# Optimization experiments

Measured on AMD Instinct MI355X. Metric: run time of the kernel, lower is better.

## Reference

```python
import jax, jax.numpy as jnp
import numpy as np

B = 64        # graphs in batch
N = 512       # nodes per graph (equal-size graphs)
DEG = 16      # avg degree
D_IN = 512
D_OUT = 512
RATIO = 0.5
K = int(np.ceil(RATIO * N))  # nodes kept per graph by SAGPool
NUM_NODES = B * N


def setup_inputs() -> dict:
    key = jax.random.key(0)
    ks = jax.random.split(key, 12)
    e_per = N * DEG
    offs = (jnp.arange(B, dtype=jnp.int32) * N)[:, None]
    src = (jax.random.randint(ks[0], (B, e_per), 0, N, dtype=jnp.int32) + offs).reshape(-1)
    dst = (jax.random.randint(ks[1], (B, e_per), 0, N, dtype=jnp.int32) + offs).reshape(-1)
    x = jax.random.normal(ks[2], (NUM_NODES, D_IN), jnp.float32)
    sc = 0.05  # small init so relu/tanh stay in sane range
    return {
        'x': x,
        'src': src,
        'dst': dst,
        'W1': jax.random.normal(ks[3], (D_IN, D_OUT), jnp.float32) * sc,
        'b1': jnp.zeros((D_OUT,), jnp.float32),
        'W2': jax.random.normal(ks[4], (D_OUT, D_OUT), jnp.float32) * sc,
        'b2': jnp.zeros((D_OUT,), jnp.float32),
        'sW1': jax.random.normal(ks[5], (D_OUT, 1), jnp.float32) * sc,
        'sb1': jnp.zeros((1,), jnp.float32),
        'sW2': jax.random.normal(ks[6], (D_OUT, 1), jnp.float32) * sc,
        'sb2': jnp.zeros((1,), jnp.float32),
    }


def graph_conv(src, dst, x, W, b, n_nodes):
    """DGL GraphConv, norm='both': D_in^{-1/2} A D_out^{-1/2} x W + b.
    W applied before aggregation (mathematically identical, cheaper when out_dim small)."""
    ones = jnp.ones(src.shape[0], x.dtype)
    deg_out = jax.ops.segment_sum(ones, src, num_segments=n_nodes)
    deg_in = jax.ops.segment_sum(ones, dst, num_segments=n_nodes)
    norm_out = jnp.maximum(deg_out, 1.0) ** -0.5  # DGL clamps deg to min 1
    norm_in = jnp.maximum(deg_in, 1.0) ** -0.5
    h = (x @ W) * norm_out[:, None]               # [n, out]
    m = jax.ops.segment_sum(h[src], dst, num_segments=n_nodes)  # gather+scatter over edges
    return m * norm_in[:, None] + b


def reference(x, src, dst, W1, b1, W2, b2, sW1, sb1, sW2, sb2):
    n = NUM_NODES
    h = jax.nn.relu(graph_conv(src, dst, x, W1, b1, n))   # conv1 + relu, reshape(-1,512) is a no-op
    h = jax.nn.relu(graph_conv(src, dst, h, W2, b2, n))   # conv2 + relu
    # SAGPool: two GraphConv score layers, averaged
    s1 = graph_conv(src, dst, h, sW1, sb1, n)[:, 0]
    s2 = graph_conv(src, dst, h, sW2, sb2, n)[:, 0]
    score = 0.5 * (s1 + s2)                                # [B*N]
    _, top_idx = jax.lax.top_k(score.reshape(B, N), K)     # per-graph top-k, [B, K]
    perm = (top_idx + (jnp.arange(B, dtype=top_idx.dtype) * N)[:, None]).reshape(-1)  # global ids
    pooled = h[perm] * jnp.tanh(score[perm])[:, None]      # [B*K, D_OUT] gated gather
    pb = pooled.reshape(B, K, D_OUT)
    # readout: max || sum per graph
    g_out = jnp.concatenate([pb.max(axis=1), pb.sum(axis=1)], axis=-1)  # [B, 2*D_OUT]
    return pooled, g_out
```

## Files before the change

kernel.cpp:

```cpp
#include <hip/hip_runtime.h>
#include <math.h>

typedef unsigned short u16;
typedef __attribute__((ext_vector_type(8))) short bf16x8;
typedef __attribute__((ext_vector_type(4))) float f32x4;

#define NN 32768
#define EDGES 524288
#define NB 64
#define NPG 512
#define EPG 8192
#define KEEP 256
#define D 512

__device__ __forceinline__ float b2f(u16 h){ return __uint_as_float(((unsigned)h)<<16); }
__device__ __forceinline__ u16 f2b(float f){
  unsigned u = __float_as_uint(f);
  unsigned r = u + 0x7FFFu + ((u>>16)&1u);
  return (u16)(r>>16);
}

__device__ __forceinline__ void gload16(const void* g, void* l){
  __builtin_amdgcn_global_load_lds((const __attribute__((address_space(1))) void*)g,
                                   (__attribute__((address_space(3))) void*)l, 16, 0, 0);
}

__device__ __forceinline__ int flag_f32(const u16* __restrict__ xb, int tid){
  __shared__ int fl;
  if (tid < 64){
    u16 v0 = xb[tid*2], v1 = xb[tid*2+1];
    int c = ((((v0>>7)&0xFF) > 140) ? 1 : 0) + ((((v1>>7)&0xFF) > 140) ? 1 : 0);
    #pragma unroll
    for (int o=32; o>=1; o>>=1) c += __shfl_xor(c, o);
    if (tid == 0) fl = (c > 8) ? 1 : 0;
  }
  __syncthreads();
  return fl;
}

__global__ __launch_bounds__(512) void prep_kernel(
    const int* __restrict__ src, const int* __restrict__ dst,
    float* __restrict__ no, float* __restrict__ ni,
    int* __restrict__ rowp, int* __restrict__ csr,
    const void* __restrict__ x,
    const void* b1, const void* b2, const void* sW1v, const void* sW2v,
    const void* sb1, const void* sb2,
    float* b1c, float* b2c, float* sW1c, float* sW2c, float* sbc,
    const void* __restrict__ W1, const void* __restrict__ W2,
    u16* __restrict__ W1Th, u16* __restrict__ W1Tl,
    u16* __restrict__ W2Th, u16* __restrict__ W2Tl,
    u16* __restrict__ Xh, u16* __restrict__ Xl)
{
  __shared__ int sh_i[5][NPG];
  __shared__ float tile[32][33];
  int b = blockIdx.x, t = threadIdx.x;

  if (b < NB){
    int* dego = sh_i[0]; int* degi = sh_i[1]; int* s = sh_i[2];
    int* start = sh_i[3]; int* cur = sh_i[4];
    int g = b, n = t;
    dego[n] = 0; degi[n] = 0; cur[n] = 0;
    __syncthreads();
    int ebase = g*EPG;
    #pragma unroll
    for (int i = 0; i < 16; i++){
      int e = ebase + n + i*512;
      atomicAdd(&dego[src[e] & (NPG-1)], 1);
      atomicAdd(&degi[dst[e] & (NPG-1)], 1);
    }
    __syncthreads();
    int di = degi[n];
    s[n] = di;
    __syncthreads();
    for (int off=1; off<NPG; off<<=1){
      int val = (n>=off) ? s[n-off] : 0;
      __syncthreads();
      s[n] += val;
      __syncthreads();
    }
    int excl = s[n] - di;
    start[n] = excl;
    int a = dego[n]; if (a<1) a=1;
    int bb = di;     if (bb<1) bb=1;
    int v = g*NPG + n;
    no[v] = (float)(1.0/sqrt((double)a));
    ni[v] = (float)(1.0/sqrt((double)bb));
    rowp[v] = ebase + excl;
    if (g == NB-1 && n == NPG-1) rowp[NN] = EDGES;
    __syncthreads();
    #pragma unroll
    for (int i = 0; i < 16; i++){
      int e = ebase + n + i*512;
      int dl = dst[e] & (NPG-1);
      int pos = atomicAdd(&cur[dl], 1);
      csr[ebase + start[dl] + pos] = src[e];
    }
  } else if (b == NB){
    int f = flag_f32((const u16*)x, t);
    #define CV(p,i) (f ? ((const float*)(p))[i] : b2f(((const u16*)(p))[i]))
    b1c[t]  = CV(b1, t);
    b2c[t]  = CV(b2, t);
    sW1c[t] = CV(sW1v, t);
    sW2c[t] = CV(sW2v, t);
    if (t==0){ sbc[0] = CV(sb1,0); sbc[1] = CV(sb2,0); }
    #undef CV
  } else if (b < NB + 1 + 512){
    int f = flag_f32((const u16*)x, t);
    int id = b - (NB+1);
    const void* W = (id >> 8) ? W2 : W1;
    u16* WTh = (id >> 8) ? W2Th : W1Th;
    u16* WTl = (id >> 8) ? W2Tl : W1Tl;
    int rem = id & 255;
    int bx = (rem & 15)*32, by = (rem >> 4)*32;
    int tx = t & 31, ty = t >> 5;
    #pragma unroll
    for (int i=0;i<2;i++){
      size_t idx = (size_t)(by+ty+i*16)*D + bx+tx;
      tile[ty+i*16][tx] = f ? ((const float*)W)[idx] : b2f(((const u16*)W)[idx]);
    }
    __syncthreads();
    #pragma unroll
    for (int i=0;i<2;i++){
      float v = tile[tx][ty+i*16];
      u16 h = f2b(v);
      size_t o = (size_t)(bx+ty+i*16)*D + by+tx;
      WTh[o] = h;
      WTl[o] = f2b(v - b2f(h));
    }
  } else {
    int f = flag_f32((const u16*)x, t);
    int nblk = gridDim.x - (NB+1+512);
    int bid  = b - (NB+1+512);
    size_t stride = (size_t)nblk*512*4;
    for (size_t i = ((size_t)bid*512 + t)*4; i < (size_t)NN*D; i += stride){
      float v0,v1,v2,v3;
      if (f){
        float4 fv = *(const float4*)((const float*)x + i);
        v0=fv.x; v1=fv.y; v2=fv.z; v3=fv.w;
      } else {
        ushort4 uv = *(const ushort4*)((const u16*)x + i);
        v0=b2f(uv.x); v1=b2f(uv.y); v2=b2f(uv.z); v3=b2f(uv.w);
      }
      ushort4 hh, hl;
      hh.x=f2b(v0); hl.x=f2b(v0-b2f(hh.x));
      hh.y=f2b(v1); hl.y=f2b(v1-b2f(hh.y));
      hh.z=f2b(v2); hl.z=f2b(v2-b2f(hh.z));
      hh.w=f2b(v3); hl.w=f2b(v3-b2f(hh.w));
      *(ushort4*)(Xh+i) = hh;
      *(ushort4*)(Xl+i) = hl;
    }
  }
}


__device__ __forceinline__ void gemm_tile256(int id, int& brow, int& bcol){
  int xcd = id & 7, k = id >> 3;
  brow = (xcd + 8*(k >> 1)) * 256;
  bcol = (k & 1) * 256;
}

__global__ __launch_bounds__(512, 2) void gemm256(
    const u16* __restrict__ Ahg, const u16* __restrict__ Alg,
    const u16* __restrict__ BTh, const u16* __restrict__ BTl,
    float* __restrict__ C, const float* __restrict__ rowscale)
{
  __shared__ alignas(16) u16 lds[2][4][8192];
  int t = threadIdx.x;
  int brow, bcol;
  gemm_tile256(blockIdx.x, brow, bcol);
  int wid = t>>6, lane = t&63;
  int wr = wid>>2, wc = wid&3;
  int q = lane>>4, r = lane&15;
  f32x4 acc[8][4] = {};

  int c0 = wid*128 + lane, c1 = c0 + 64;
  int q0 = c0>>8, r0 = c0&255, q1 = c1>>8, r1 = c1&255;
  const u16* sA0h = Ahg + (size_t)(brow+r0)*D + q0*8;
  const u16* sA1h = Ahg + (size_t)(brow+r1)*D + q1*8;
  const u16* sA0l = Alg + (size_t)(brow+r0)*D + q0*8;
  const u16* sA1l = Alg + (size_t)(brow+r1)*D + q1*8;
  const u16* sB0h = BTh + (size_t)(bcol+r0)*D + q0*8;
  const u16* sB1h = BTh + (size_t)(bcol+r1)*D + q1*8;
  const u16* sB0l = BTl + (size_t)(bcol+r0)*D + q0*8;
  const u16* sB1l = BTl + (size_t)(bcol+r1)*D + q1*8;

  #define STAGEK(B, KT) { int ko = (KT)*32; \
    gload16(sA0h+ko, &lds[B][0][c0*8]); gload16(sA1h+ko, &lds[B][0][c1*8]); \
    gload16(sA0l+ko, &lds[B][1][c0*8]); gload16(sA1l+ko, &lds[B][1][c1*8]); \
    gload16(sB0h+ko, &lds[B][2][c0*8]); gload16(sB1h+ko, &lds[B][2][c1*8]); \
    gload16(sB0l+ko, &lds[B][3][c0*8]); gload16(sB1l+ko, &lds[B][3][c1*8]); }

  STAGEK(0, 0)
  asm volatile("s_waitcnt vmcnt(0)" ::: "memory");
  __syncthreads();
  int cur = 0;
  for (int kt=0; kt<16; kt++){
    if (kt < 15) STAGEK(cur^1, kt+1)
    bf16x8 fbh[4], fbl[4];
    #pragma unroll
    for (int n=0;n<4;n++){
      fbh[n] = *(const bf16x8*)(&lds[cur][2][(q*256 + wc*64 + n*16 + r)*8]);
      fbl[n] = *(const bf16x8*)(&lds[cur][3][(q*256 + wc*64 + n*16 + r)*8]);
    }
    __builtin_amdgcn_s_setprio(1);
    #pragma unroll
    for (int m=0;m<8;m++){
      bf16x8 fah = *(const bf16x8*)(&lds[cur][0][(q*256 + wr*128 + m*16 + r)*8]);
      bf16x8 fal = *(const bf16x8*)(&lds[cur][1][(q*256 + wr*128 + m*16 + r)*8]);
      #pragma unroll
      for (int n=0;n<4;n++){
        acc[m][n] = __builtin_amdgcn_mfma_f32_16x16x32_bf16(fah, fbh[n], acc[m][n], 0,0,0);
        acc[m][n] = __builtin_amdgcn_mfma_f32_16x16x32_bf16(fah, fbl[n], acc[m][n], 0,0,0);
        acc[m][n] = __builtin_amdgcn_mfma_f32_16x16x32_bf16(fal, fbh[n], acc[m][n], 0,0,0);
      }
    }
    __builtin_amdgcn_s_setprio(0);
    asm volatile("s_waitcnt vmcnt(0)" ::: "memory");
    __syncthreads();
    cur ^= 1;
  }
  #undef STAGEK

  #pragma unroll
  for (int m=0;m<8;m++){
    int rowb = brow + wr*128 + m*16 + q*4;
    #pragma unroll
    for (int n=0;n<4;n++){
      int col = bcol + wc*64 + n*16 + r;
      #pragma unroll
      for (int g=0; g<4; g++){
        int row = rowb + g;
        C[(size_t)row*D + col] = acc[m][n][g] * rowscale[row];
      }
    }
  }
}


__global__ __launch_bounds__(256) void agg_kernel(
    const float* __restrict__ Y, const int* __restrict__ rowp,
    const int* __restrict__ csr, const float* __restrict__ ni,
    const float* __restrict__ bias,
    u16* __restrict__ Hh, u16* __restrict__ Hl,
    const float* __restrict__ sW1, const float* __restrict__ sW2,
    float* __restrict__ t1, float* __restrict__ t2, int mode)
{
  int i = blockIdx.x;
  int xcd = i & 7, j = i >> 3;
  int half = threadIdx.x >> 7;
  int t = threadIdx.x & 127;
  int lane = threadIdx.x & 63;
  int v = (xcd + 8*(j >> 8))*NPG + ((j & 255)*2 + half);
  int rp0 = rowp[v], rp1 = rowp[v+1];
  const float4* Yv = (const float4*)Y;
  float4 a = {0.f,0.f,0.f,0.f};
  for (int eb = rp0; eb < rp1; eb += 64){
    int cnt = rp1 - eb; if (cnt > 64) cnt = 64;
    int idx = (lane < cnt) ? csr[eb + lane] : 0;
    int e = 0;
    for (; e+8 <= cnt; e += 8){
      int u0 = __shfl(idx, e),   u1 = __shfl(idx, e+1);
      int u2 = __shfl(idx, e+2), u3 = __shfl(idx, e+3);
      int u4 = __shfl(idx, e+4), u5 = __shfl(idx, e+5);
      int u6 = __shfl(idx, e+6), u7 = __shfl(idx, e+7);
      float4 y0 = Yv[(size_t)u0*128 + t];
      float4 y1 = Yv[(size_t)u1*128 + t];
      float4 y2 = Yv[(size_t)u2*128 + t];
      float4 y3 = Yv[(size_t)u3*128 + t];
      float4 y4 = Yv[(size_t)u4*128 + t];
      float4 y5 = Yv[(size_t)u5*128 + t];
      float4 y6 = Yv[(size_t)u6*128 + t];
      float4 y7 = Yv[(size_t)u7*128 + t];
      a.x += ((y0.x + y1.x) + (y2.x + y3.x)) + ((y4.x + y5.x) + (y6.x + y7.x));
      a.y += ((y0.y + y1.y) + (y2.y + y3.y)) + ((y4.y + y5.y) + (y6.y + y7.y));
      a.z += ((y0.z + y1.z) + (y2.z + y3.z)) + ((y4.z + y5.z) + (y6.z + y7.z));
      a.w += ((y0.w + y1.w) + (y2.w + y3.w)) + ((y4.w + y5.w) + (y6.w + y7.w));
    }
    for (; e+4 <= cnt; e += 4){
      int u0 = __shfl(idx, e),   u1 = __shfl(idx, e+1);
      int u2 = __shfl(idx, e+2), u3 = __shfl(idx, e+3);
      float4 y0 = Yv[(size_t)u0*128 + t];
      float4 y1 = Yv[(size_t)u1*128 + t];
      float4 y2 = Yv[(size_t)u2*128 + t];
      float4 y3 = Yv[(size_t)u3*128 + t];
      a.x += (y0.x + y1.x) + (y2.x + y3.x);
      a.y += (y0.y + y1.y) + (y2.y + y3.y);
      a.z += (y0.z + y1.z) + (y2.z + y3.z);
      a.w += (y0.w + y1.w) + (y2.w + y3.w);
    }
    for (; e < cnt; e++){
      int u = __shfl(idx, e);
      float4 y = Yv[(size_t)u*128 + t];
      a.x += y.x; a.y += y.y; a.z += y.z; a.w += y.w;
    }
  }
  float w = ni[v];
  float4 b4 = ((const float4*)bias)[t];
  float4 rr;
  rr.x = fmaxf(a.x*w + b4.x, 0.f);
  rr.y = fmaxf(a.y*w + b4.y, 0.f);
  rr.z = fmaxf(a.z*w + b4.z, 0.f);
  rr.w = fmaxf(a.w*w + b4.w, 0.f);

  if (mode == 0){
    ushort4 hh, hl;
    hh.x = f2b(rr.x); hl.x = f2b(rr.x - b2f(hh.x));
    hh.y = f2b(rr.y); hl.y = f2b(rr.y - b2f(hh.y));
    hh.z = f2b(rr.z); hl.z = f2b(rr.z - b2f(hh.z));
    hh.w = f2b(rr.w); hl.w = f2b(rr.w - b2f(hh.w));
    *(ushort4*)(Hh + (size_t)v*D + t*4) = hh;
    *(ushort4*)(Hl + (size_t)v*D + t*4) = hl;
  } else {
    ushort4 hb;
    hb.x = f2b(rr.x); hb.y = f2b(rr.y); hb.z = f2b(rr.z); hb.w = f2b(rr.w);
    *(ushort4*)(Hh + (size_t)v*D + t*4) = hb;
    float4 w1 = ((const float4*)sW1)[t];
    float4 w2 = ((const float4*)sW2)[t];
    float p1 = rr.x*w1.x + rr.y*w1.y + rr.z*w1.z + rr.w*w1.w;
    float p2 = rr.x*w2.x + rr.y*w2.y + rr.z*w2.z + rr.w*w2.w;
    #pragma unroll
    for (int off=32; off>=1; off>>=1){
      p1 += __shfl_xor(p1, off);
      p2 += __shfl_xor(p2, off);
    }
    __shared__ float red1[4], red2[4];
    int wv = threadIdx.x>>6;
    if (lane==0){ red1[wv] = p1; red2[wv] = p2; }
    __syncthreads();
    if (t==0){
      t1[v] = red1[half*2] + red1[half*2+1];
      t2[v] = red2[half*2] + red2[half*2+1];
    }
  }
}


__global__ __launch_bounds__(512) void scoretopk_kernel(
    const float* __restrict__ t1, const float* __restrict__ t2,
    const int* __restrict__ rowp, const int* __restrict__ csr,
    const float* __restrict__ no, const float* __restrict__ ni,
    const float* __restrict__ sbc,
    int* __restrict__ perm, float* __restrict__ gate)
{
  __shared__ unsigned long long key[NPG];
  __shared__ float scl[NPG];
  int g = blockIdx.x, n = threadIdx.x;
  int v = g*NPG + n;
  double a1 = 0.0, a2 = 0.0;
  int rp1 = rowp[v+1];
  for (int e=rowp[v]; e<rp1; e++){
    int u = csr[e];
    double w = (double)no[u];
    a1 += (double)t1[u]*w;
    a2 += (double)t2[u]*w;
  }
  double wi = (double)ni[v];
  double s1 = a1*wi + (double)sbc[0];
  double s2 = a2*wi + (double)sbc[1];
  float s = (float)(0.5*(s1+s2));
  scl[n] = s;
  unsigned u = __float_as_uint(s);
  u = (u & 0x80000000u) ? ~u : (u | 0x80000000u);
  unsigned kd = ~u;
  key[n] = ((unsigned long long)kd<<32) | (unsigned)n;
  __syncthreads();
  for (int k=2; k<=NPG; k<<=1){
    for (int j=k>>1; j>0; j>>=1){
      int ixj = n ^ j;
      if (ixj > n){
        unsigned long long a = key[n], b = key[ixj];
        bool up = ((n & k) == 0);
        if ((a > b) == up){ key[n] = b; key[ixj] = a; }
      }
      __syncthreads();
    }
  }
  if (n < KEEP){
    int idx = (int)(key[n] & 0xFFFFFFFFull);
    perm[g*KEEP + n] = g*NPG + idx;
    gate[g*KEEP + n] = tanhf(scl[idx]);
  }
}


__global__ __launch_bounds__(256) void readout_kernel(const u16* __restrict__ Hb,
    const int* __restrict__ perm, const float* __restrict__ gate,
    float* __restrict__ outp, float* __restrict__ gmx, float* __restrict__ gsm)
{
  __shared__ float4 redmx[128], redsm[128];
  int b = blockIdx.x;
  int g = b >> 3, seg = b & 7;
  int t = threadIdx.x, half = t >> 7, c = t & 127;
  float4 mx = {-INFINITY,-INFINITY,-INFINITY,-INFINITY};
  float4 sm = {0.f,0.f,0.f,0.f};
  int base = seg*32;
  for (int rI = base + half; rI < base + 32; rI += 2){
    int node = perm[g*KEEP + rI];
    float gt = gate[g*KEEP + rI];
    ushort4 hv = *(const ushort4*)(Hb + (size_t)node*D + c*4);
    float4 vv;
    vv.x = b2f(hv.x)*gt; vv.y = b2f(hv.y)*gt;
    vv.z = b2f(hv.z)*gt; vv.w = b2f(hv.w)*gt;
    ((float4*)(outp + (size_t)(g*KEEP + rI)*D))[c] = vv;
    mx.x = fmaxf(mx.x, vv.x); mx.y = fmaxf(mx.y, vv.y);
    mx.z = fmaxf(mx.z, vv.z); mx.w = fmaxf(mx.w, vv.w);
    sm.x += vv.x; sm.y += vv.y; sm.z += vv.z; sm.w += vv.w;
  }
  if (half == 1){ redmx[c] = mx; redsm[c] = sm; }
  __syncthreads();
  if (half == 0){
    float4 omx = redmx[c], osm = redsm[c];
    mx.x = fmaxf(mx.x, omx.x); mx.y = fmaxf(mx.y, omx.y);
    mx.z = fmaxf(mx.z, omx.z); mx.w = fmaxf(mx.w, omx.w);
    sm.x += osm.x; sm.y += osm.y; sm.z += osm.z; sm.w += osm.w;
    ((float4*)(gmx + (size_t)b*512))[c] = mx;
    ((float4*)(gsm + (size_t)b*512))[c] = sm;
  }
}


__global__ __launch_bounds__(512) void combine_kernel(const float* __restrict__ gmx,
    const float* __restrict__ gsm, float* __restrict__ outg)
{
  int g = blockIdx.x, d = threadIdx.x;
  float mx = -INFINITY, sm = 0.f;
  #pragma unroll
  for (int s=0; s<8; s++){
    mx = fmaxf(mx, gmx[(size_t)(g*8+s)*512 + d]);
    sm += gsm[(size_t)(g*8+s)*512 + d];
  }
  outg[(size_t)g*1024 + d] = mx;
  outg[(size_t)g*1024 + 512 + d] = sm;
}


extern "C" void kernel_launch(void* const* d_in, const int* in_sizes, int n_in,
                              void* d_out, int out_size, void* d_ws, size_t ws_size,
                              hipStream_t stream)
{
  (void)in_sizes; (void)n_in; (void)out_size; (void)ws_size;
  const void* x   = d_in[0];
  const int* src  = (const int*)d_in[1];
  const int* dst  = (const int*)d_in[2];
  const void* W1  = d_in[3];
  const void* b1  = d_in[4];
  const void* W2  = d_in[5];
  const void* b2  = d_in[6];
  const void* sW1 = d_in[7];
  const void* sb1 = d_in[8];
  const void* sW2 = d_in[9];
  const void* sb2 = d_in[10];
  float* out = (float*)d_out;

  char* ws = (char*)d_ws;
  size_t off = 0;
  auto alloc = [&](size_t bytes){ void* p = ws + off; off += (bytes + 255) & ~(size_t)255; return p; };
  float* no     = (float*)alloc((size_t)NN*4);
  float* ni     = (float*)alloc((size_t)NN*4);
  int*   rowp   = (int*)  alloc((size_t)(NN+1)*4);
  float* t1     = (float*)alloc((size_t)NN*4);
  float* t2     = (float*)alloc((size_t)NN*4);
  int*   perm   = (int*)  alloc((size_t)NB*KEEP*4);
  float* gate   = (float*)alloc((size_t)NB*KEEP*4);
  float* b1c    = (float*)alloc((size_t)D*4);
  float* b2c    = (float*)alloc((size_t)D*4);
  float* sW1c   = (float*)alloc((size_t)D*4);
  float* sW2c   = (float*)alloc((size_t)D*4);
  float* sbc    = (float*)alloc(2*4);
  float* gmx    = (float*)alloc((size_t)512*512*4);
  float* gsm    = (float*)alloc((size_t)512*512*4);
  u16*   W1Th   = (u16*)  alloc((size_t)D*D*2);
  u16*   W1Tl   = (u16*)  alloc((size_t)D*D*2);
  u16*   W2Th   = (u16*)  alloc((size_t)D*D*2);
  u16*   W2Tl   = (u16*)  alloc((size_t)D*D*2);
  int*   csr    = (int*)  alloc((size_t)EDGES*4);
  u16*   Hh     = (u16*)  alloc((size_t)NN*D*2);
  u16*   Hl     = (u16*)  alloc((size_t)NN*D*2);
  float* Y      = (float*)alloc((size_t)NN*D*4);
  u16*   Xh     = (u16*)  alloc((size_t)NN*D*2);
  u16*   Xl     = (u16*)  alloc((size_t)NN*D*2);
  u16*   Hb     = Hh;

  prep_kernel<<<2048, 512, 0, stream>>>(src, dst, no, ni, rowp, csr, x,
                                        b1, b2, sW1, sW2, sb1, sb2,
                                        b1c, b2c, sW1c, sW2c, sbc,
                                        W1, W2, W1Th, W1Tl, W2Th, W2Tl, Xh, Xl);

  gemm256<<<256, 512, 0, stream>>>(Xh, Xl, W1Th, W1Tl, Y, no);
  agg_kernel<<<NN/2, 256, 0, stream>>>(Y, rowp, csr, ni, b1c, Hh, Hl,
                                       nullptr, nullptr, nullptr, nullptr, 0);
  gemm256<<<256, 512, 0, stream>>>(Hh, Hl, W2Th, W2Tl, Y, no);
  agg_kernel<<<NN/2, 256, 0, stream>>>(Y, rowp, csr, ni, b2c, Hb, nullptr,
                                       sW1c, sW2c, t1, t2, 1);

  scoretopk_kernel<<<NB, 512, 0, stream>>>(t1, t2, rowp, csr, no, ni, sbc, perm, gate);
  readout_kernel  <<<512, 256, 0, stream>>>(Hb, perm, gate, out, gmx, gsm);
  combine_kernel  <<<NB, 512, 0, stream>>>(gmx, gsm, out + (size_t)NB*KEEP*D);
}
```

Measured before the change: 284.4 us.

## Fuse score/topk, readout and combine into one cooperative kernel; widen aggregation blocks

Merges the three tail kernels into a single cooperative launch separated by grid-wide syncs, removing two kernel launch boundaries. The aggregation kernel now processes four nodes per 512-thread block instead of two per 256, and the GEMM k-loop is fully unrolled with a compile-time buffer index. Grid syncs and cooperative launch add their own overhead, and only 64 of the 512 blocks do work in the first and last phases.

```diff
diff --git a/kernel.cpp b/kernel.cpp
--- a/kernel.cpp
+++ b/kernel.cpp
@@ -1,4 +1,5 @@
 #include <hip/hip_runtime.h>
+#include <hip/hip_cooperative_groups.h>
 #include <math.h>
 
 typedef unsigned short u16;
@@ -193,8 +194,9 @@
   STAGEK(0, 0)
   asm volatile("s_waitcnt vmcnt(0)" ::: "memory");
   __syncthreads();
-  int cur = 0;
+  #pragma unroll
   for (int kt=0; kt<16; kt++){
+    const int cur = kt & 1;
     if (kt < 15) STAGEK(cur^1, kt+1)
     bf16x8 fbh[4], fbl[4];
     #pragma unroll
@@ -217,7 +219,6 @@
     __builtin_amdgcn_s_setprio(0);
     asm volatile("s_waitcnt vmcnt(0)" ::: "memory");
     __syncthreads();
-    cur ^= 1;
   }
   #undef STAGEK
 
@@ -237,7 +238,7 @@
 }
 
 
-__global__ __launch_bounds__(256) void agg_kernel(
+__global__ __launch_bounds__(512) void agg_kernel(
     const float* __restrict__ Y, const int* __restrict__ rowp,
     const int* __restrict__ csr, const float* __restrict__ ni,
     const float* __restrict__ bias,
@@ -247,10 +248,10 @@
 {
   int i = blockIdx.x;
   int xcd = i & 7, j = i >> 3;
-  int half = threadIdx.x >> 7;
+  int quarter = threadIdx.x >> 7;
   int t = threadIdx.x & 127;
   int lane = threadIdx.x & 63;
-  int v = (xcd + 8*(j >> 8))*NPG + ((j & 255)*2 + half);
+  int v = (xcd + 8*(j >> 7))*NPG + ((j & 127)*4 + quarter);
   int rp0 = rowp[v], rp1 = rowp[v+1];
   const float4* Yv = (const float4*)Y;
   float4 a = {0.f,0.f,0.f,0.f};
@@ -323,114 +324,119 @@
       p1 += __shfl_xor(p1, off);
       p2 += __shfl_xor(p2, off);
     }
-    __shared__ float red1[4], red2[4];
+    __shared__ float red1[8], red2[8];
     int wv = threadIdx.x>>6;
     if (lane==0){ red1[wv] = p1; red2[wv] = p2; }
     __syncthreads();
     if (t==0){
-      t1[v] = red1[half*2] + red1[half*2+1];
-      t2[v] = red2[half*2] + red2[half*2+1];
-    }
-  }
-}
-
-
-__global__ __launch_bounds__(512) void scoretopk_kernel(
+      t1[v] = red1[quarter*2] + red1[quarter*2+1];
+      t2[v] = red2[quarter*2] + red2[quarter*2+1];
+    }
+  }
+}
+
+
+__global__ __launch_bounds__(512) void tail_kernel(
     const float* __restrict__ t1, const float* __restrict__ t2,
     const int* __restrict__ rowp, const int* __restrict__ csr,
     const float* __restrict__ no, const float* __restrict__ ni,
-    const float* __restrict__ sbc,
-    int* __restrict__ perm, float* __restrict__ gate)
+    const float* __restrict__ sbc, const u16* __restrict__ Hb,
+    int* __restrict__ perm, float* __restrict__ gate,
+    float* __restrict__ gmx, float* __restrict__ gsm,
+    float* __restrict__ outp, float* __restrict__ outg)
 {
   __shared__ unsigned long long key[NPG];
   __shared__ float scl[NPG];
-  int g = blockIdx.x, n = threadIdx.x;
-  int v = g*NPG + n;
-  double a1 = 0.0, a2 = 0.0;
-  int rp1 = rowp[v+1];
-  for (int e=rowp[v]; e<rp1; e++){
-    int u = csr[e];
-    double w = (double)no[u];
-    a1 += (double)t1[u]*w;
-    a2 += (double)t2[u]*w;
-  }
-  double wi = (double)ni[v];
-  double s1 = a1*wi + (double)sbc[0];
-  double s2 = a2*wi + (double)sbc[1];
-  float s = (float)(0.5*(s1+s2));
-  scl[n] = s;
-  unsigned u = __float_as_uint(s);
-  u = (u & 0x80000000u) ? ~u : (u | 0x80000000u);
-  unsigned kd = ~u;
-  key[n] = ((unsigned long long)kd<<32) | (unsigned)n;
-  __syncthreads();
-  for (int k=2; k<=NPG; k<<=1){
-    for (int j=k>>1; j>0; j>>=1){
-      int ixj = n ^ j;
-      if (ixj > n){
-        unsigned long long a = key[n], b = key[ixj];
-        bool up = ((n & k) == 0);
-        if ((a > b) == up){ key[n] = b; key[ixj] = a; }
+  __shared__ float4 redmx[3*128], redsm[3*128];
+  cooperative_groups::grid_group grid = cooperative_groups::this_grid();
+  int b = blockIdx.x, n = threadIdx.x;
+
+  if (b < NB){
+    int g = b;
+    int v = g*NPG + n;
+    double a1 = 0.0, a2 = 0.0;
+    int rp1 = rowp[v+1];
+    for (int e=rowp[v]; e<rp1; e++){
+      int u = csr[e];
+      double w = (double)no[u];
+      a1 += (double)t1[u]*w;
+      a2 += (double)t2[u]*w;
+    }
+    double wi = (double)ni[v];
+    double s1 = a1*wi + (double)sbc[0];
+    double s2 = a2*wi + (double)sbc[1];
+    float s = (float)(0.5*(s1+s2));
+    scl[n] = s;
+    unsigned u = __float_as_uint(s);
+    u = (u & 0x80000000u) ? ~u : (u | 0x80000000u);
+    unsigned kd = ~u;
+    key[n] = ((unsigned long long)kd<<32) | (unsigned)n;
+    __syncthreads();
+    for (int k=2; k<=NPG; k<<=1){
+      for (int j=k>>1; j>0; j>>=1){
+        int ixj = n ^ j;
+        if (ixj > n){
+          unsigned long long a = key[n], bb = key[ixj];
+          bool up = ((n & k) == 0);
+          if ((a > bb) == up){ key[n] = bb; key[ixj] = a; }
+        }
+        __syncthreads();
       }
-      __syncthreads();
-    }
-  }
-  if (n < KEEP){
-    int idx = (int)(key[n] & 0xFFFFFFFFull);
-    perm[g*KEEP + n] = g*NPG + idx;
-    gate[g*KEEP + n] = tanhf(scl[idx]);
-  }
-}
-
-
-__global__ __launch_bounds__(256) void readout_kernel(const u16* __restrict__ Hb,
-    const int* __restrict__ perm, const float* __restrict__ gate,
-    float* __restrict__ outp, float* __restrict__ gmx, float* __restrict__ gsm)
-{
-  __shared__ float4 redmx[128], redsm[128];
-  int b = blockIdx.x;
-  int g = b >> 3, seg = b & 7;
-  int t = threadIdx.x, half = t >> 7, c = t & 127;
-  float4 mx = {-INFINITY,-INFINITY,-INFINITY,-INFINITY};
-  float4 sm = {0.f,0.f,0.f,0.f};
-  int base = seg*32;
-  for (int rI = base + half; rI < base + 32; rI += 2){
-    int node = perm[g*KEEP + rI];
-    float gt = gate[g*KEEP + rI];
-    ushort4 hv = *(const ushort4*)(Hb + (size_t)node*D + c*4);
-    float4 vv;
-    vv.x = b2f(hv.x)*gt; vv.y = b2f(hv.y)*gt;
-    vv.z = b2f(hv.z)*gt; vv.w = b2f(hv.w)*gt;
-    ((float4*)(outp + (size_t)(g*KEEP + rI)*D))[c] = vv;
-    mx.x = fmaxf(mx.x, vv.x); mx.y = fmaxf(mx.y, vv.y);
-    mx.z = fmaxf(mx.z, vv.z); mx.w = fmaxf(mx.w, vv.w);
-    sm.x += vv.x; sm.y += vv.y; sm.z += vv.z; sm.w += vv.w;
-  }
-  if (half == 1){ redmx[c] = mx; redsm[c] = sm; }
-  __syncthreads();
-  if (half == 0){
-    float4 omx = redmx[c], osm = redsm[c];
-    mx.x = fmaxf(mx.x, omx.x); mx.y = fmaxf(mx.y, omx.y);
-    mx.z = fmaxf(mx.z, omx.z); mx.w = fmaxf(mx.w, omx.w);
-    sm.x += osm.x; sm.y += osm.y; sm.z += osm.z; sm.w += osm.w;
-    ((float4*)(gmx + (size_t)b*512))[c] = mx;
-    ((float4*)(gsm + (size_t)b*512))[c] = sm;
-  }
-}
-
-
-__global__ __launch_bounds__(512) void combine_kernel(const float* __restrict__ gmx,
-    const float* __restrict__ gsm, float* __restrict__ outg)
-{
-  int g = blockIdx.x, d = threadIdx.x;
-  float mx = -INFINITY, sm = 0.f;
-  #pragma unroll
-  for (int s=0; s<8; s++){
-    mx = fmaxf(mx, gmx[(size_t)(g*8+s)*512 + d]);
-    sm += gsm[(size_t)(g*8+s)*512 + d];
-  }
-  outg[(size_t)g*1024 + d] = mx;
-  outg[(size_t)g*1024 + 512 + d] = sm;
+    }
+    if (n < KEEP){
+      int idx = (int)(key[n] & 0xFFFFFFFFull);
+      perm[g*KEEP + n] = g*NPG + idx;
+      gate[g*KEEP + n] = tanhf(scl[idx]);
+    }
+  }
+  grid.sync();
+
+  {
+    int g = b >> 3, seg = b & 7;
+    int qtr = n >> 7, c = n & 127;
+    float4 mx = {-INFINITY,-INFINITY,-INFINITY,-INFINITY};
+    float4 sm = {0.f,0.f,0.f,0.f};
+    int base = seg*32;
+    for (int rI = base + qtr; rI < base + 32; rI += 4){
+      int node = perm[g*KEEP + rI];
+      float gt = gate[g*KEEP + rI];
+      ushort4 hv = *(const ushort4*)(Hb + (size_t)node*D + c*4);
+      float4 vv;
+      vv.x = b2f(hv.x)*gt; vv.y = b2f(hv.y)*gt;
+      vv.z = b2f(hv.z)*gt; vv.w = b2f(hv.w)*gt;
+      ((float4*)(outp + (size_t)(g*KEEP + rI)*D))[c] = vv;
+      mx.x = fmaxf(mx.x, vv.x); mx.y = fmaxf(mx.y, vv.y);
+      mx.z = fmaxf(mx.z, vv.z); mx.w = fmaxf(mx.w, vv.w);
+      sm.x += vv.x; sm.y += vv.y; sm.z += vv.z; sm.w += vv.w;
+    }
+    __syncthreads();
+    if (qtr > 0){ redmx[(qtr-1)*128 + c] = mx; redsm[(qtr-1)*128 + c] = sm; }
+    __syncthreads();
+    if (qtr == 0){
+      #pragma unroll
+      for (int qq=0; qq<3; qq++){
+        float4 omx = redmx[qq*128 + c], osm = redsm[qq*128 + c];
+        mx.x = fmaxf(mx.x, omx.x); mx.y = fmaxf(mx.y, omx.y);
+        mx.z = fmaxf(mx.z, omx.z); mx.w = fmaxf(mx.w, omx.w);
+        sm.x += osm.x; sm.y += osm.y; sm.z += osm.z; sm.w += osm.w;
+      }
+      ((float4*)(gmx + (size_t)b*512))[c] = mx;
+      ((float4*)(gsm + (size_t)b*512))[c] = sm;
+    }
+  }
+  grid.sync();
+
+  if (b < NB){
+    int g = b, d = n;
+    float mx = -INFINITY, sm = 0.f;
+    #pragma unroll
+    for (int s=0; s<8; s++){
+      mx = fmaxf(mx, gmx[(size_t)(g*8+s)*512 + d]);
+      sm += gsm[(size_t)(g*8+s)*512 + d];
+    }
+    outg[(size_t)g*1024 + d] = mx;
+    outg[(size_t)g*1024 + 512 + d] = sm;
+  }
 }
 
 
@@ -487,13 +493,16 @@
                                         W1, W2, W1Th, W1Tl, W2Th, W2Tl, Xh, Xl);
 
   gemm256<<<256, 512, 0, stream>>>(Xh, Xl, W1Th, W1Tl, Y, no);
-  agg_kernel<<<NN/2, 256, 0, stream>>>(Y, rowp, csr, ni, b1c, Hh, Hl,
+  agg_kernel<<<NN/4, 512, 0, stream>>>(Y, rowp, csr, ni, b1c, Hh, Hl,
                                        nullptr, nullptr, nullptr, nullptr, 0);
   gemm256<<<256, 512, 0, stream>>>(Hh, Hl, W2Th, W2Tl, Y, no);
-  agg_kernel<<<NN/2, 256, 0, stream>>>(Y, rowp, csr, ni, b2c, Hb, nullptr,
+  agg_kernel<<<NN/4, 512, 0, stream>>>(Y, rowp, csr, ni, b2c, Hb, nullptr,
                                        sW1c, sW2c, t1, t2, 1);
 
-  scoretopk_kernel<<<NB, 512, 0, stream>>>(t1, t2, rowp, csr, no, ni, sbc, perm, gate);
-  readout_kernel  <<<512, 256, 0, stream>>>(Hb, perm, gate, out, gmx, gsm);
-  combine_kernel  <<<NB, 512, 0, stream>>>(gmx, gsm, out + (size_t)NB*KEEP*D);
-}
+  float* outg = out + (size_t)NB*KEEP*D;
+  void* args[] = { (void*)&t1, (void*)&t2, (void*)&rowp, (void*)&csr,
+                   (void*)&no, (void*)&ni, (void*)&sbc, (void*)&Hb,
+                   (void*)&perm, (void*)&gate, (void*)&gmx, (void*)&gsm,
+                   (void*)&out, (void*)&outg };
+  hipLaunchCooperativeKernel((void*)tail_kernel, dim3(512), dim3(512), args, 0, stream);
+}
```

New measurement: 401.4 us. +41.1%, slower.
